# Performance work log

Hardware: AMD Instinct MI355X
Metric: run time of the kernel (lower is better)

Reference implementation:

```python
import jax, jax.numpy as jnp
import numpy as np
from jax import lax

EPS = 1e-5

def _sign(x):
    # sign with sign(0)=+1, as used in XNOR-style binarization
    return jnp.where(x >= 0, 1.0, -1.0).astype(x.dtype)

def binarize(x):
    # straight-through estimator: forward = sign(x), backward = identity
    return x + lax.stop_gradient(_sign(x) - x)

def batchnorm(x, p):
    # p: [4, C] rows = (gamma, beta, running_mean, running_var); eval-mode BN
    g, b, m, v = p[0], p[1], p[2], p[3]
    shape = (1, -1) + (1,) * (x.ndim - 2)
    inv = g / jnp.sqrt(v + EPS)
    return (x - m.reshape(shape)) * inv.reshape(shape) + b.reshape(shape)

def conv2d(x, w):
    return lax.conv_general_dilated(x, w, window_strides=(1, 1), padding='VALID',
                                    dimension_numbers=('NCHW', 'OIHW', 'NCHW'))

def maxpool2(x):
    return lax.reduce_window(x, -jnp.inf, lax.max, (1, 1, 2, 2), (1, 1, 2, 2), 'VALID')

def hardtanh(x):
    return jnp.clip(x, -1.0, 1.0)


def setup_inputs() -> dict:
    key = jax.random.key(0)
    ks = jax.random.split(key, 16)
    B = 16384
    x = jax.random.normal(ks[0], (B, 3, 22, 22), jnp.float32)
    w1 = jax.random.normal(ks[1], (32, 3, 3, 3), jnp.float32) * 0.1
    w2 = jax.random.normal(ks[2], (32, 32, 3, 3), jnp.float32) * 0.1
    w3 = jax.random.normal(ks[3], (64, 32, 3, 3), jnp.float32) * 0.1
    w_fc1 = jax.random.normal(ks[4], (128, 64), jnp.float32) * 0.1
    w_fc2 = jax.random.normal(ks[5], (2, 128), jnp.float32) * 0.1
    w_fc3 = jax.random.normal(ks[6], (4, 128), jnp.float32) * 0.1

    def make_bn(k, c):
        k1, k2, k3, k4 = jax.random.split(k, 4)
        gamma = jax.random.uniform(k1, (c,), jnp.float32, 0.5, 1.5)
        beta = jax.random.normal(k2, (c,), jnp.float32) * 0.1
        mean = jax.random.normal(k3, (c,), jnp.float32) * 0.1
        var = jax.random.uniform(k4, (c,), jnp.float32, 0.5, 1.5)
        return jnp.stack([gamma, beta, mean, var])  # [4, C]

    bn1 = make_bn(ks[7], 32)
    bn2 = make_bn(ks[8], 32)
    bn3 = make_bn(ks[9], 64)
    bn4 = make_bn(ks[10], 128)
    bn5 = make_bn(ks[11], 2)
    bn6 = make_bn(ks[12], 4)
    return {'x': x, 'w1': w1, 'w2': w2, 'w3': w3, 'w_fc1': w_fc1, 'w_fc2': w_fc2,
            'w_fc3': w_fc3, 'bn1': bn1, 'bn2': bn2, 'bn3': bn3, 'bn4': bn4,
            'bn5': bn5, 'bn6': bn6}


def reference(x, w1, w2, w3, w_fc1, w_fc2, w_fc3, bn1, bn2, bn3, bn4, bn5, bn6):
    # binary=True, binarize_input=True, bitwidth=input_bitwidth=1:
    # every BinarizeConv2d/BinarizeLinear binarizes both its input and weights.
    h = hardtanh(batchnorm(conv2d(binarize(x), binarize(w1)), bn1))   # [B,32,20,20]
    h = maxpool2(h)                                                    # [B,32,10,10]
    h = hardtanh(batchnorm(conv2d(binarize(h), binarize(w2)), bn2))   # [B,32,8,8]
    h = maxpool2(h)                                                    # [B,32,4,4]
    h = hardtanh(batchnorm(conv2d(binarize(h), binarize(w3)), bn3))   # [B,64,2,2]
    h = maxpool2(h)                                                    # [B,64,1,1]
    h = h.reshape(-1, 64)                                              # [B,64]
    h = hardtanh(batchnorm(binarize(h) @ binarize(w_fc1).T, bn4))      # [B,128]
    out1 = jax.nn.softmax(batchnorm(h @ w_fc2.T, bn5), axis=1)         # [B,2]
    out2 = batchnorm(h @ w_fc3.T, bn6)                                 # [B,4]
    return (out1, out2)
```

## Files before the change

kernel.cpp:

```cpp
#include <hip/hip_runtime.h>
#include <cstdint>
#include <cmath>

typedef int  v4i  __attribute__((ext_vector_type(4)));
typedef int  v16i __attribute__((ext_vector_type(16)));
typedef unsigned int u32x4 __attribute__((ext_vector_type(4)));

#define OFF_W1   0
#define OFF_T1   32
#define OFF_W3   384
#define OFF_T3   960
#define OFF_WFC1 1024
#define OFF_A4   1280
#define OFF_C4   1408
#define OFF_WF2  1536
#define OFF_WF3  1792
#define OFF_BN5  2304
#define OFF_BN6  2308
#define OFF_B2   2560
#define OFF_T2C  4864

__device__ __forceinline__ int thr_neg(double nterms, double g, double b, double m, double v) {
    double inv = g / sqrt(v + 1e-5);
    double t = m - b / inv;
    double thr = floor((nterms - t) * 0.5);
    if (thr < -2147000000.0) thr = -2147000000.0;
    if (thr >  2147000000.0) thr =  2147000000.0;
    return -((int)thr + 1);
}

__device__ __forceinline__ int thr_c_neg(double g, double b, double m, double v) {
    double inv = g / sqrt(v + 1e-5);
    double t = m - b / inv;
    double ct = ceil(t);
    if (ct < -2147000000.0) ct = -2147000000.0;
    if (ct >  2147000000.0) ct =  2147000000.0;
    return -(int)ct;
}

__global__ void k_prep(const float* __restrict__ w1, const float* __restrict__ w2,
                       const float* __restrict__ w3, const float* __restrict__ wfc1,
                       const float* __restrict__ wfc2, const float* __restrict__ wfc3,
                       const float* __restrict__ bn1, const float* __restrict__ bn2,
                       const float* __restrict__ bn3, const float* __restrict__ bn4,
                       const float* __restrict__ bn5, const float* __restrict__ bn6,
                       unsigned int* __restrict__ ws) {
    __shared__ float stage[9216];
    int t = threadIdx.x;
    int blk = blockIdx.x;
    float* wsf = (float*)ws;
    int*   wsi = (int*)ws;

    if (blk == 0) {
        for (int i = t; i < 864; i += 256) stage[i] = w1[i];
        __syncthreads();
        if (t < 32) {
            unsigned int bits = 0;
            for (int j = 0; j < 27; ++j) bits |= (stage[t*27+j] >= 0.f ? 1u : 0u) << j;
            ws[OFF_W1 + t] = bits;
            wsi[OFF_T1 + t]  = thr_neg(27.0, bn1[t], bn1[32+t], bn1[64+t], bn1[96+t]);
            wsi[OFF_T2C + t] = thr_c_neg(bn2[t], bn2[32+t], bn2[64+t], bn2[96+t]);
        }
        for (int i = t; i < 256; i += 256) wsf[OFF_WF2 + i] = wfc2[i];
        for (int i = t; i < 512; i += 256) wsf[OFF_WF3 + i] = wfc3[i];
        if (t < 2) {
            float g = bn5[t], b = bn5[2+t], m = bn5[4+t], v = bn5[6+t];
            float inv = g / sqrtf(v + 1e-5f);
            wsf[OFF_BN5 + t]     = inv;
            wsf[OFF_BN5 + 2 + t] = b - m * inv;
        }
        if (t >= 4 && t < 8) {
            int j = t - 4;
            float g = bn6[j], b = bn6[4+j], m = bn6[8+j], v = bn6[12+j];
            float inv = g / sqrtf(v + 1e-5f);
            wsf[OFF_BN6 + j]     = inv;
            wsf[OFF_BN6 + 4 + j] = b - m * inv;
        }
    } else if (blk == 1) {
        for (int i = t; i < 9216; i += 256) stage[i] = w2[i];
        __syncthreads();
        for (int idx = t; idx < 2304; idx += 256) {
            int s   = idx >> 8;
            int rem = idx & 255;
            int l   = rem >> 2;
            int reg = rem & 3;
            int och = l & 31;
            int icb = ((l >> 5) << 4) + (reg << 2);
            unsigned int wv = 0;
            #pragma unroll
            for (int j = 0; j < 4; ++j) {
                int ic = icb + j;
                unsigned int by = (stage[(och*32 + ic)*9 + s] >= 0.f) ? 0x01u : 0xFFu;
                wv |= by << (8*j);
            }
            ws[OFF_B2 + idx] = wv;
        }
    } else if (blk == 2 || blk == 3) {
        int base = (blk - 2) * 9216;
        for (int i = t; i < 9216; i += 256) stage[i] = w3[base + i];
        __syncthreads();
        for (int idx = t; idx < 288; idx += 256) {
            int o = idx / 9, k = idx - o*9;
            unsigned int bits = 0;
            for (int i = 0; i < 32; ++i)
                bits |= (stage[(o*32+i)*9 + k] >= 0.f ? 1u : 0u) << i;
            ws[OFF_W3 + base/32 + idx] = bits;
        }
    } else {
        for (int i = t; i < 8192; i += 256) stage[i] = wfc1[i];
        __syncthreads();
        if (t < 128) {
            unsigned int lo = 0, hi = 0;
            for (int j = 0; j < 32; ++j) lo |= (stage[t*64+j]    >= 0.f ? 1u : 0u) << j;
            for (int j = 0; j < 32; ++j) hi |= (stage[t*64+32+j] >= 0.f ? 1u : 0u) << j;
            ws[OFF_WFC1 + 2*t]     = lo;
            ws[OFF_WFC1 + 2*t + 1] = hi;
            float g = bn4[t], b = bn4[128+t], m = bn4[256+t], v = bn4[384+t];
            float inv = g / sqrtf(v + 1e-5f);
            wsf[OFF_A4 + t] = -2.f * inv;
            wsf[OFF_C4 + t] = (64.f - m) * inv + b;
        }
        if (t >= 128 && t < 192) {
            int j = t - 128;
            wsi[OFF_T3 + j] = thr_neg(288.0, bn3[j], bn3[64+j], bn3[128+j], bn3[192+j]);
        }
    }
}

#define WSTRIDE 916
__global__ __launch_bounds__(256) void k_main(const float* __restrict__ x,
                                              const unsigned int* __restrict__ ws,
                                              float* __restrict__ out, int B) {
    __shared__ __align__(16) unsigned int s_u[4 * WSTRIDE];

    const int tid = threadIdx.x & 63;
    const int wid = threadIdx.x >> 6;
    const int b   = blockIdx.x * 4 + wid;
    if (b >= B) return;
    const float* wsf = (const float*)ws;
    const int*   wsi = (const int*)ws;

    unsigned int* bytes = s_u + wid * WSTRIDE;
    unsigned int* inrow = bytes;
    unsigned int* c1    = bytes + 66;
    unsigned int* pb1   = bytes + 800;
    unsigned int* pb2   = bytes + 900;

    for (int r = tid; r < 66; r += 64) {
        int c = r / 22, y = r - c*22;
        const float2* p = (const float2*)(x + ((size_t)b*3 + c)*484 + (size_t)y*22);
        unsigned int bits = 0;
        #pragma unroll
        for (int j = 0; j < 11; ++j) {
            float2 v = p[j];
            bits |= (v.x >= 0.f ? 1u : 0u) << (2*j);
            bits |= (v.y >= 0.f ? 1u : 0u) << (2*j+1);
        }
        inrow[r] = bits;
    }
    __builtin_amdgcn_wave_barrier();

    for (int pos = tid; pos < 400; pos += 64) {
        int y = pos / 20, xx = pos - y*20;
        unsigned int g = 0;
        #pragma unroll
        for (int c = 0; c < 3; ++c)
            #pragma unroll
            for (int dy = 0; dy < 3; ++dy)
                g |= ((inrow[c*22 + y + dy] >> xx) & 7u) << (c*9 + dy*3);
        unsigned int word = 0;
        #pragma unroll
        for (int o = 31; o >= 0; --o) {
            unsigned int s = (unsigned int)(__popc(g ^ ws[OFF_W1 + o]) + wsi[OFF_T1 + o]);
            word = __builtin_amdgcn_alignbit(word, s, 31);
        }
        c1[pos] = word;
    }
    __builtin_amdgcn_wave_barrier();

    for (int p = tid; p < 100; p += 64) {
        int py = p / 10, px = p - py*10;
        int base = (2*py)*20 + 2*px;
        pb1[p] = c1[base] | c1[base+1] | c1[base+20] | c1[base+21];
    }
    __builtin_amdgcn_wave_barrier();

    #pragma unroll
    for (int i = 0; i < 4; ++i) {
        int ch = tid + 64*i;
        if (ch < 200) {
            unsigned int w = pb1[ch >> 1];
            int sh = (ch & 1) << 4;
            u32x4 o;
            #pragma unroll
            for (int j = 0; j < 4; ++j) {
                unsigned int nib = (w >> (sh + 4*j)) & 0xFu;
                unsigned int sp  = (nib * 0x204081u) & 0x01010101u;
                o[j] = __builtin_amdgcn_perm(0u, 0x000001FFu, sp);
            }
            *(u32x4*)(bytes + ch*4) = o;
        }
    }
    __builtin_amdgcn_wave_barrier();

    {
        int nthr2 = wsi[OFF_T2C + (tid & 31)];
        const v4i* __restrict__ Bfr = (const v4i*)(ws + OFF_B2);
        #pragma unroll
        for (int tile = 0; tile < 2; ++tile) {
            int r   = tid & 31;
            int gq  = tile*8 + (r >> 2);
            int sub = r & 3;
            int y   = ((gq >> 2) << 1) + (sub >> 1);
            int x   = ((gq & 3) << 1) + (sub & 1);
            const v4i* __restrict__ Ab = (const v4i*)(bytes + (y*10 + x)*8 + ((tid >> 5) << 2));
            v16i acc;
            #pragma unroll
            for (int j = 0; j < 16; ++j) acc[j] = nthr2;
            #pragma unroll
            for (int s = 0; s < 9; ++s) {
                int dy = s / 3, dx = s - dy*3;
                v4i a  = Ab[(dy*10 + dx)*2];
                v4i bf = Bfr[s*64 + tid];
                acc = __builtin_amdgcn_mfma_i32_32x32x32_i8(a, bf, acc, 0, 0, 0);
            }
            #pragma unroll
            for (int g = 0; g < 4; ++g) {
                int m0 = acc[4*g]   > acc[4*g+1] ? acc[4*g]   : acc[4*g+1];
                int m1 = acc[4*g+2] > acc[4*g+3] ? acc[4*g+2] : acc[4*g+3];
                int mx = m0 > m1 ? m0 : m1;
                unsigned long long bal = __ballot(mx >= 0);
                if (tid == 0) {
                    pb2[tile*8 + 2*g]     = (unsigned int)bal;
                    pb2[tile*8 + 2*g + 1] = (unsigned int)(bal >> 32);
                }
            }
        }
    }
    __builtin_amdgcn_wave_barrier();

    unsigned long long b3 = 0;
    {
        unsigned int bb[16];
        #pragma unroll
        for (int i = 0; i < 16; ++i) bb[i] = pb2[i];
        unsigned int w3r[9];
        #pragma unroll
        for (int k = 0; k < 9; ++k) w3r[k] = ws[OFF_W3 + tid*9 + k];
        int negt = wsi[OFF_T3 + tid];
        unsigned int oracc = 0;
        #pragma unroll
        for (int py = 0; py < 2; ++py)
            #pragma unroll
            for (int px = 0; px < 2; ++px) {
                int s = negt;
                #pragma unroll
                for (int dy = 0; dy < 3; ++dy)
                    #pragma unroll
                    for (int dx = 0; dx < 3; ++dx)
                        s += __popc(bb[(py+dy)*4 + px + dx] ^ w3r[dy*3+dx]);
                oracc |= (unsigned int)s;
            }
        b3 = __ballot((int)oracc < 0);
    }

    float h0, h1;
    {
        const unsigned long long* wfc1b = (const unsigned long long*)(ws + OFF_WFC1);
        int pc0 = __popcll(b3 ^ wfc1b[tid]);
        int pc1 = __popcll(b3 ^ wfc1b[tid + 64]);
        float p0 = fmaf((float)pc0, wsf[OFF_A4 + tid],      wsf[OFF_C4 + tid]);
        float p1 = fmaf((float)pc1, wsf[OFF_A4 + tid + 64], wsf[OFF_C4 + tid + 64]);
        h0 = fminf(1.f, fmaxf(-1.f, p0));
        h1 = fminf(1.f, fmaxf(-1.f, p1));
    }

    {
        float part[6];
        #pragma unroll
        for (int j = 0; j < 2; ++j)
            part[j] = h0 * wsf[OFF_WF2 + j*128 + tid] + h1 * wsf[OFF_WF2 + j*128 + 64 + tid];
        #pragma unroll
        for (int j = 0; j < 4; ++j)
            part[2+j] = h0 * wsf[OFF_WF3 + j*128 + tid] + h1 * wsf[OFF_WF3 + j*128 + 64 + tid];
        #pragma unroll
        for (int off = 32; off; off >>= 1) {
            #pragma unroll
            for (int j = 0; j < 6; ++j)
                part[j] += __shfl_xor(part[j], off);
        }
        if (tid < 6) {
            if (tid < 2) {
                float y0 = part[0]*wsf[OFF_BN5+0] + wsf[OFF_BN5+2];
                float y1 = part[1]*wsf[OFF_BN5+1] + wsf[OFF_BN5+3];
                float mx = fmaxf(y0, y1);
                float e0 = expf(y0 - mx), e1 = expf(y1 - mx);
                float r  = 1.f / (e0 + e1);
                out[(size_t)b*2 + tid] = (tid == 0 ? e0 : e1) * r;
            } else {
                int j = tid - 2;
                out[(size_t)B*2 + (size_t)b*4 + j] = part[2+j]*wsf[OFF_BN6+j] + wsf[OFF_BN6+4+j];
            }
        }
    }
}

extern "C" void kernel_launch(void* const* d_in, const int* in_sizes, int n_in,
                              void* d_out, int out_size, void* d_ws, size_t ws_size,
                              hipStream_t stream) {
    const float* x    = (const float*)d_in[0];
    const float* w1   = (const float*)d_in[1];
    const float* w2   = (const float*)d_in[2];
    const float* w3   = (const float*)d_in[3];
    const float* wfc1 = (const float*)d_in[4];
    const float* wfc2 = (const float*)d_in[5];
    const float* wfc3 = (const float*)d_in[6];
    const float* bn1  = (const float*)d_in[7];
    const float* bn2  = (const float*)d_in[8];
    const float* bn3  = (const float*)d_in[9];
    const float* bn4  = (const float*)d_in[10];
    const float* bn5  = (const float*)d_in[11];
    const float* bn6  = (const float*)d_in[12];
    unsigned int* ws  = (unsigned int*)d_ws;
    float* out        = (float*)d_out;
    int B = in_sizes[0] / 1452;

    k_prep<<<5, 256, 0, stream>>>(w1, w2, w3, wfc1, wfc2, wfc3,
                                  bn1, bn2, bn3, bn4, bn5, bn6, ws);
    k_main<<<(B + 3) / 4, 256, 0, stream>>>(x, ws, out, B);
}
```

Before: 184.3 us.

## Preload conv2 MFMA weights into registers and keep pooled bits in VGPRs

```diff
diff --git a/kernel.cpp b/kernel.cpp
--- a/kernel.cpp
+++ b/kernel.cpp
@@ -127,10 +127,10 @@
     }
 }
 
-#define WSTRIDE 916
-__global__ __launch_bounds__(256) void k_main(const float* __restrict__ x,
-                                              const unsigned int* __restrict__ ws,
-                                              float* __restrict__ out, int B) {
+#define WSTRIDE 900
+__global__ __launch_bounds__(256, 4) void k_main(const float* __restrict__ x,
+                                                 const unsigned int* __restrict__ ws,
+                                                 float* __restrict__ out, int B) {
     __shared__ __align__(16) unsigned int s_u[4 * WSTRIDE];
 
     const int tid = threadIdx.x & 63;
@@ -144,7 +144,6 @@
     unsigned int* inrow = bytes;
     unsigned int* c1    = bytes + 66;
     unsigned int* pb1   = bytes + 800;
-    unsigned int* pb2   = bytes + 900;
 
     for (int r = tid; r < 66; r += 64) {
         int c = r / 22, y = r - c*22;
@@ -160,6 +159,14 @@
     }
     __builtin_amdgcn_wave_barrier();
 
+    v4i Breg[9];
+    {
+        const v4i* __restrict__ Bfr = (const v4i*)(ws + OFF_B2);
+        #pragma unroll
+        for (int s = 0; s < 9; ++s) Breg[s] = Bfr[s*64 + tid];
+    }
+    const int nthr2 = wsi[OFF_T2C + (tid & 31)];
+
     for (int pos = tid; pos < 400; pos += 64) {
         int y = pos / 20, xx = pos - y*20;
         unsigned int g = 0;
@@ -187,10 +194,12 @@
 
     #pragma unroll
     for (int i = 0; i < 4; ++i) {
-        int ch = tid + 64*i;
-        if (ch < 200) {
-            unsigned int w = pb1[ch >> 1];
-            int sh = (ch & 1) << 4;
+        int c2 = tid + 64*i;
+        if (c2 < 200) {
+            int hi  = (c2 >= 100) ? 1 : 0;
+            int pos = c2 - hi*100;
+            unsigned int w = pb1[pos];
+            int sh = hi << 4;
             u32x4 o;
             #pragma unroll
             for (int j = 0; j < 4; ++j) {
@@ -198,14 +207,19 @@
                 unsigned int sp  = (nib * 0x204081u) & 0x01010101u;
                 o[j] = __builtin_amdgcn_perm(0u, 0x000001FFu, sp);
             }
-            *(u32x4*)(bytes + ch*4) = o;
+            *(u32x4*)(bytes + c2*4) = o;
         }
     }
     __builtin_amdgcn_wave_barrier();
 
-    {
-        int nthr2 = wsi[OFF_T2C + (tid & 31)];
-        const v4i* __restrict__ Bfr = (const v4i*)(ws + OFF_B2);
+    unsigned int w3r[9];
+    #pragma unroll
+    for (int k = 0; k < 9; ++k) w3r[k] = ws[OFF_W3 + tid*9 + k];
+    const int negt3 = wsi[OFF_T3 + tid];
+
+    unsigned int pb2w[16];
+    {
+        const int hi = tid >> 5;
         #pragma unroll
         for (int tile = 0; tile < 2; ++tile) {
             int r   = tid & 31;
@@ -213,52 +227,43 @@
             int sub = r & 3;
             int y   = ((gq >> 2) << 1) + (sub >> 1);
             int x   = ((gq & 3) << 1) + (sub & 1);
-            const v4i* __restrict__ Ab = (const v4i*)(bytes + (y*10 + x)*8 + ((tid >> 5) << 2));
+            const v4i* __restrict__ Ab = (const v4i*)(bytes + (hi*100 + y*10 + x)*4);
             v16i acc;
             #pragma unroll
             for (int j = 0; j < 16; ++j) acc[j] = nthr2;
+            __builtin_amdgcn_s_setprio(1);
             #pragma unroll
             for (int s = 0; s < 9; ++s) {
                 int dy = s / 3, dx = s - dy*3;
-                v4i a  = Ab[(dy*10 + dx)*2];
-                v4i bf = Bfr[s*64 + tid];
-                acc = __builtin_amdgcn_mfma_i32_32x32x32_i8(a, bf, acc, 0, 0, 0);
-            }
+                v4i a = Ab[dy*10 + dx];
+                acc = __builtin_amdgcn_mfma_i32_32x32x32_i8(a, Breg[s], acc, 0, 0, 0);
+            }
+            __builtin_amdgcn_s_setprio(0);
             #pragma unroll
             for (int g = 0; g < 4; ++g) {
                 int m0 = acc[4*g]   > acc[4*g+1] ? acc[4*g]   : acc[4*g+1];
                 int m1 = acc[4*g+2] > acc[4*g+3] ? acc[4*g+2] : acc[4*g+3];
                 int mx = m0 > m1 ? m0 : m1;
                 unsigned long long bal = __ballot(mx >= 0);
-                if (tid == 0) {
-                    pb2[tile*8 + 2*g]     = (unsigned int)bal;
-                    pb2[tile*8 + 2*g + 1] = (unsigned int)(bal >> 32);
-                }
-            }
-        }
-    }
-    __builtin_amdgcn_wave_barrier();
+                pb2w[tile*8 + 2*g]     = (unsigned int)bal;
+                pb2w[tile*8 + 2*g + 1] = (unsigned int)(bal >> 32);
+            }
+        }
+    }
 
     unsigned long long b3 = 0;
     {
-        unsigned int bb[16];
-        #pragma unroll
-        for (int i = 0; i < 16; ++i) bb[i] = pb2[i];
-        unsigned int w3r[9];
-        #pragma unroll
-        for (int k = 0; k < 9; ++k) w3r[k] = ws[OFF_W3 + tid*9 + k];
-        int negt = wsi[OFF_T3 + tid];
         unsigned int oracc = 0;
         #pragma unroll
         for (int py = 0; py < 2; ++py)
             #pragma unroll
             for (int px = 0; px < 2; ++px) {
-                int s = negt;
+                int s = negt3;
                 #pragma unroll
                 for (int dy = 0; dy < 3; ++dy)
                     #pragma unroll
                     for (int dx = 0; dx < 3; ++dx)
-                        s += __popc(bb[(py+dy)*4 + px + dx] ^ w3r[dy*3+dx]);
+                        s += __popc(pb2w[(py+dy)*4 + px + dx] ^ w3r[dy*3+dx]);
                 oracc |= (unsigned int)s;
             }
         b3 = __ballot((int)oracc < 0);
```

Result: faster. 179.9 us (-2.4%).
